# Performance work log

Measured on AMD Instinct MI355X. Metric: run time of the kernel, lower is better.

The kernel has to match this reference:

```python
import jax, jax.numpy as jnp
import numpy as np

B, N_HEADS, KEY_DIM, ATTN_RATIO, RES, DIM = 8, 12, 64, 4, 32, 768
D = ATTN_RATIO * KEY_DIM          # per-head v dim = 256
DH = N_HEADS * D                  # 3072
QKV_OUT = N_HEADS * (2 * KEY_DIM + D)  # 4608
N = RES * RES                     # 1024 tokens
TH = 0.99
WBITS, ABITS, PGABITS = 8, 8, 4


def quantize(x, bits):
    # TorchQuantize: round(x * 2^(b-1)) / 2^(b-1) with straight-through estimator
    s = jnp.asarray(2.0 ** (bits - 1), x.dtype)
    q = jnp.round(x * s) / s
    return x + jax.lax.stop_gradient(q - x)


def ste_greater_than(x, th):
    # GreaterThan: hard (x > th) forward, identity gradient
    hard = (x > th).astype(x.dtype)
    return x + jax.lax.stop_gradient(hard - x)


def hardswish(x):
    return x * jnp.clip(x + 3.0, 0.0, 6.0) / 6.0


def _make_bias_idxs(res):
    pts = np.stack(np.meshgrid(np.arange(res), np.arange(res), indexing='ij'), -1).reshape(-1, 2)
    off = np.abs(pts[:, None, :] - pts[None, :, :])          # [N,N,2]
    key = off[..., 0] * res + off[..., 1]
    uniq, inv = np.unique(key, return_inverse=True)
    return inv.reshape(res * res, res * res).astype(np.int32), len(uniq)


def setup_inputs() -> dict:
    key = jax.random.key(0)
    ks = jax.random.split(key, 8)
    bias_idxs_np, n_uniq = _make_bias_idxs(RES)
    return {
        "x": jax.random.normal(ks[0], (B, N, DIM), jnp.float32),
        "qkv_w": jax.random.normal(ks[1], (QKV_OUT, DIM), jnp.float32) * (DIM ** -0.5),
        "qkv_g": jnp.ones((QKV_OUT,), jnp.float32),
        "qkv_b": jnp.zeros((QKV_OUT,), jnp.float32),
        "proj_w": jax.random.normal(ks[2], (DIM, DH), jnp.float32) * (DH ** -0.5),
        "proj_g": jnp.ones((DIM,), jnp.float32),
        "proj_b": jnp.zeros((DIM,), jnp.float32),
        "attn_biases": jax.random.normal(ks[3], (N_HEADS, n_uniq), jnp.float32) * 0.02,
        "bias_idxs": jnp.asarray(bias_idxs_np),
    }


def reference(x, qkv_w, qkv_g, qkv_b, proj_w, proj_g, proj_b, attn_biases, bias_idxs):
    Bq, Nq, C = x.shape
    scale = KEY_DIM ** -0.5
    # QLinear qkv (8-bit act/weight) followed by fused BN affine (Linear_BN)
    h = quantize(x, ABITS) @ quantize(qkv_w, WBITS).T
    h = h * qkv_g + qkv_b                                     # [B,N,QKV_OUT]
    h = quantize(h, ABITS)
    h = h.reshape(Bq, Nq, N_HEADS, 2 * KEY_DIM + D).transpose(0, 2, 1, 3)  # [B,H,N,*]
    q, k, v = h[..., :KEY_DIM], h[..., KEY_DIM:2 * KEY_DIM], h[..., 2 * KEY_DIM:]
    bias = attn_biases[:, bias_idxs]                          # [H,N,N]
    # MSB (low-precision) predictive attention -> gating mask
    q_msb = quantize(q, PGABITS)
    k_msb = quantize(k, PGABITS)
    attn_msb = jnp.einsum('bhnd,bhmd->bhnm', q_msb, k_msb) * scale + bias
    attn_msb = jax.nn.softmax(attn_msb, axis=-1)
    mask = ste_greater_than(attn_msb, TH)                     # [B,H,N,N]
    # Full-precision attention, threshold-gated (ena_schedule=False)
    attn = jnp.einsum('bhnd,bhmd->bhnm', q, k) * scale + bias
    attn = jax.nn.softmax(attn * mask, axis=-1)
    attn = quantize(attn, ABITS)
    out = jnp.einsum('bhnm,bhmd->bhnd', attn, v)              # [B,H,N,D]
    out = out.transpose(0, 2, 1, 3).reshape(Bq, Nq, DH)
    out = hardswish(out)                                      # proj = Seq(act, Linear_BN)
    out = quantize(out, ABITS) @ quantize(proj_w, WBITS).T
    out = out * proj_g + proj_b                               # [B,N,DIM]
    return out
```

## Files before the change

### kernel.cpp

```cpp
#include <hip/hip_runtime.h>

typedef _Float16 f16;
typedef _Float16 f16x8 __attribute__((ext_vector_type(8)));
typedef _Float16 f16x4 __attribute__((ext_vector_type(4)));
typedef float    f32x4 __attribute__((ext_vector_type(4)));
typedef int      i32x4 __attribute__((ext_vector_type(4)));

#define MFMA16(a,b,c) __builtin_amdgcn_mfma_f32_16x16x32_f16((a),(b),(c),0,0,0)
#define MFMAI8(a,b,c) __builtin_amdgcn_mfma_i32_16x16x64_i8((a),(b),(c),0,0,0)
#define AS1(p) ((const __attribute__((address_space(1))) void*)(p))
#define AS3(p) ((__attribute__((address_space(3))) void*)(p))

constexpr int   NH   = 12;
constexpr int   SEQ  = 1024;
constexpr float INV128 = 1.0f/128.0f;
constexpr int   ECAP = 98304;
constexpr float THR_NOT = -4.5948f;

__device__ __forceinline__ float q8f(float x){ return rintf(x*128.0f)*INV128; }
__device__ __forceinline__ float q4f(float x){ return rintf(x*8.0f)*0.125f; }

__global__ __launch_bounds__(256) void prelude(
    const float* __restrict__ x, const float* __restrict__ qkv_w,
    float* __restrict__ out, const float* __restrict__ pb,
    const float* __restrict__ biases, int NU,
    f16* __restrict__ xq, f16* __restrict__ wqk,
    float* __restrict__ Bh, int* __restrict__ cnt2)
{
    const int b = blockIdx.x, t = threadIdx.x;
    if (b < 6144){
        int i = (b*256 + t)*4;
        float4 v = *(const float4*)(x + i);
        f16x4 o;
        o[0]=(f16)q8f(v.x); o[1]=(f16)q8f(v.y); o[2]=(f16)q8f(v.z); o[3]=(f16)q8f(v.w);
        *(f16x4*)(xq + i) = o;
    } else if (b < 7296){
        int i = ((b-6144)*256 + t)*4;
        int r = i / 768, col = i - r*768;
        int srow = (r>>7)*384 + (r&127);
        float4 v = *(const float4*)(qkv_w + (size_t)srow*768 + col);
        f16x4 o;
        o[0]=(f16)q8f(v.x); o[1]=(f16)q8f(v.y); o[2]=(f16)q8f(v.z); o[3]=(f16)q8f(v.w);
        *(f16x4*)(wqk + i) = o;
    } else if (b < 13440){
        int i = ((b-7296)*256 + t)*4;
        int c = i % 768;
        float4 v = { pb[c], pb[c+1], pb[c+2], pb[c+3] };
        *(float4*)(out + i) = v;
    } else {
        int h = b - 13440;
        float m = 0.f;
        for (int i = t; i < NU; i += 256) m = fmaxf(m, fabsf(biases[h*NU + i]));
        #pragma unroll
        for (int d=32; d>=1; d>>=1) m = fmaxf(m, __shfl_xor(m, d));
        __shared__ float s[4];
        if ((t&63)==0) s[t>>6] = m;
        __syncthreads();
        if (t==0){
            Bh[h] = fmaxf(fmaxf(s[0],s[1]), fmaxf(s[2],s[3]));
            if (h==0) *cnt2 = 0;
        }
    }
}

__global__ __launch_bounds__(256, 2) void gemm_qk(
    const f16* __restrict__ Aq, const f16* __restrict__ Wqk,
    const float* __restrict__ g, const float* __restrict__ bb,
    signed char* __restrict__ Qi, signed char* __restrict__ Ki)
{
    __shared__ f16 As[2][128][64];
    __shared__ f16 Bs[2][192][64];
    const int t = threadIdx.x;
    const int bid = blockIdx.x;
    const int xcd = bid & 7, idx = bid >> 3;
    const int mt  = xcd*8 + (idx >> 3);
    const int nt  = idx & 7;
    const int row0 = mt*128, col0 = nt*192;
    const int w = t>>6, lane = t&63;
    const int wr = (w>>1)*64, wc = (w&1)*96;
    const int lr = lane&15, lg = lane>>4;

    const int rloc  = lane>>3;
    const int sgran = (lane&7) ^ rloc;
    const f16* Abase = Aq  + (size_t)(row0 + w*32 + rloc)*768 + sgran*8;
    const f16* Bbase = Wqk + (size_t)(col0 + w*48 + rloc)*768 + sgran*8;

    f32x4 acc[4][6] = {};

#define STAGE(buf, kt) { \
    const int ko = (kt)*64; \
    __builtin_amdgcn_global_load_lds(AS1(Abase + (size_t) 0*768 + ko), AS3(&As[buf][w*32 +  0][0]), 16, 0, 0); \
    __builtin_amdgcn_global_load_lds(AS1(Abase + (size_t) 8*768 + ko), AS3(&As[buf][w*32 +  8][0]), 16, 0, 0); \
    __builtin_amdgcn_global_load_lds(AS1(Abase + (size_t)16*768 + ko), AS3(&As[buf][w*32 + 16][0]), 16, 0, 0); \
    __builtin_amdgcn_global_load_lds(AS1(Abase + (size_t)24*768 + ko), AS3(&As[buf][w*32 + 24][0]), 16, 0, 0); \
    __builtin_amdgcn_global_load_lds(AS1(Bbase + (size_t) 0*768 + ko), AS3(&Bs[buf][w*48 +  0][0]), 16, 0, 0); \
    __builtin_amdgcn_global_load_lds(AS1(Bbase + (size_t) 8*768 + ko), AS3(&Bs[buf][w*48 +  8][0]), 16, 0, 0); \
    __builtin_amdgcn_global_load_lds(AS1(Bbase + (size_t)16*768 + ko), AS3(&Bs[buf][w*48 + 16][0]), 16, 0, 0); \
    __builtin_amdgcn_global_load_lds(AS1(Bbase + (size_t)24*768 + ko), AS3(&Bs[buf][w*48 + 24][0]), 16, 0, 0); \
    __builtin_amdgcn_global_load_lds(AS1(Bbase + (size_t)32*768 + ko), AS3(&Bs[buf][w*48 + 32][0]), 16, 0, 0); \
    __builtin_amdgcn_global_load_lds(AS1(Bbase + (size_t)40*768 + ko), AS3(&Bs[buf][w*48 + 40][0]), 16, 0, 0); }

    STAGE(0, 0)

    for (int kt = 0; kt < 12; kt++){
        __builtin_amdgcn_s_barrier();
        if (kt < 11){
            STAGE((kt+1)&1, kt+1)
            asm volatile("s_waitcnt vmcnt(10)" ::: "memory");
        } else {
            asm volatile("s_waitcnt vmcnt(0)" ::: "memory");
        }
        __builtin_amdgcn_s_barrier();

        const int bsel = kt & 1;
        #pragma unroll
        for (int kk=0; kk<2; kk++){
            const int slot = ((kk*4 + lg) ^ (lr&7))*8;
            f16x8 af[4], bf[6];
            #pragma unroll
            for (int i=0;i<4;i++)
                af[i] = *(const f16x8*)&As[bsel][wr + i*16 + lr][slot];
            #pragma unroll
            for (int j=0;j<6;j++)
                bf[j] = *(const f16x8*)&Bs[bsel][wc + j*16 + lr][slot];
            __builtin_amdgcn_s_setprio(1);
            #pragma unroll
            for (int i=0;i<4;i++)
                #pragma unroll
                for (int j=0;j<6;j++)
                    acc[i][j] = MFMA16(af[i], bf[j], acc[i][j]);
            __builtin_amdgcn_s_setprio(0);
        }
    }
#undef STAGE

    #pragma unroll
    for (int j=0;j<6;j++){
        int c = col0 + wc + j*16 + lr;
        int head = c >> 7, rr = c & 127;
        int gcol = head*384 + rr;
        float gg = g[gcol], bv = bb[gcol];
        signed char* dst = (rr < 64) ? Qi : Ki;
        int dcol = rr & 63;
        #pragma unroll
        for (int i=0;i<4;i++){
            #pragma unroll
            for (int r=0;r<4;r++){
                int grow = row0 + wr + i*16 + lg*4 + r;
                float h = __fadd_rn(__fmul_rn(acc[i][j][r], gg), bv);
                int iv = (int)rintf(q8f(h)*8.0f);
                int bq = grow >> 10, n = grow & 1023;
                dst[((size_t)(bq*NH + head)*SEQ + n)*64 + dcol] = (signed char)iv;
            }
        }
    }
}

__global__ __launch_bounds__(256) void pass_a(
    const signed char* __restrict__ Qi, const signed char* __restrict__ Ki,
    const float* __restrict__ Bh,
    int* __restrict__ cnt2, int2* __restrict__ amb)
{
    __shared__ signed char Ks[128][64];

    const int t = threadIdx.x;
    const int bid = blockIdx.x;
    const int wg  = (bid & 7)*192 + (bid >> 3);
    const int bh  = wg >> 4;
    const int qt  = wg & 15;
    const int n0 = qt*64;
    const int lane = t&63, w = t>>6;
    const int lr = lane&15, lg = lane>>4;

    const float thr512 = (THR_NOT + 2.0f*Bh[bh % NH] + 1e-4f) * 512.0f;

    const signed char* qp = Qi + ((size_t)bh*SEQ + n0 + w*16 + lr)*64;
    const i32x4 aq = *(const i32x4*)(qp + lg*16);

    const signed char* Kb = Ki + (size_t)bh*SEQ*64;

    int mx[4], m2[4];
    #pragma unroll
    for (int r=0;r<4;r++){ mx[r] = -(1<<30); m2[r] = -(1<<30); }

    for (int kb = 0; kb < SEQ; kb += 128){
        __syncthreads();
        for (int s = t; s < 512; s += 256){
            int r = s>>2, gsw = s&3;
            int src = (gsw ^ (r&3))*16;
            *(i32x4*)&Ks[r][gsw*16] = *(const i32x4*)(Kb + (size_t)(kb + r)*64 + src);
        }
        __syncthreads();
        #pragma unroll
        for (int ct=0; ct<8; ct++){
            const int row = ct*16 + lr;
            i32x4 bq = *(const i32x4*)&Ks[row][(lg ^ (lr&3))*16];
            i32x4 c = {0,0,0,0};
            c = MFMAI8(aq, bq, c);
            #pragma unroll
            for (int r=0;r<4;r++){
                int sc = c[r];
                int om = mx[r];
                asm("v_med3_i32 %0, %1, %2, %3" : "=v"(m2[r]) : "v"(sc), "v"(m2[r]), "v"(om));
                mx[r] = max(om, sc);
            }
        }
    }

    #pragma unroll
    for (int r=0;r<4;r++){
        int mxv = mx[r], m2v = m2[r];
        #pragma unroll
        for (int d=1; d<16; d<<=1){
            int mo  = __shfl_xor(mxv, d);
            int m2o = __shfl_xor(m2v, d);
            int sec = max(min(mxv, mo), (mxv >= mo) ? m2v : m2o);
            mxv = max(mxv, mo);
            m2v = sec;
        }
        if (lr == 0){
            if ((float)(m2v - mxv) < thr512){
                int n = n0 + w*16 + lg*4 + r;
                int pos = atomicAdd(cnt2, 1);
                if (pos < ECAP) amb[pos] = make_int2((bh<<10) | n, 0);
            }
        }
    }
}

__global__ __launch_bounds__(256) void tail_kernel(
    const signed char* __restrict__ Qi, const signed char* __restrict__ Ki,
    const float* __restrict__ biases, int NU,
    const f16* __restrict__ xq, const f16* __restrict__ wqk,
    const float* __restrict__ qkv_w,
    const float* __restrict__ g, const float* __restrict__ bb,
    const float* __restrict__ proj_w, const float* __restrict__ pg,
    const int* __restrict__ cnt2, const int2* __restrict__ amb,
    float* __restrict__ out)
{
    __shared__ int   qr[64];
    __shared__ float rmax[4], rsum[4];
    __shared__ int   rarg[4];
    __shared__ float xr_n[768], xr_m[768];
    __shared__ float qs[64], ks[64];
    __shared__ float hq[256];
    __shared__ float s_as;
    __shared__ int   s_ms, s_flag;
    int total = *cnt2; if (total > ECAP) total = ECAP;
    const int t = threadIdx.x;
    for (int e = blockIdx.x; e < total; e += gridDim.x){
        int2 a = amb[e];
        int bh = a.x>>10, n = a.x&1023;
        int h = bh % NH, b = bh / NH;
        __syncthreads();
        if (t < 64) qr[t] = (int)Qi[((size_t)bh*SEQ + n)*64 + t];
        __syncthreads();

        int rn = n>>5, cnn = n&31;
        float lmax = -3e38f; int larg = 0; float lsc[4];
        #pragma unroll
        for (int j=0;j<4;j++){
            int m = t + j*256;
            const signed char* kp = &Ki[((size_t)bh*SEQ + m)*64];
            int d = 0;
            for (int u=0; u<64; u++) d += qr[u]*(int)kp[u];
            int idx = __builtin_abs(rn-(m>>5))*32 + __builtin_abs(cnn-(m&31));
            lsc[j] = (float)d*(1.0f/512.0f) + biases[h*NU + idx];
            if (lsc[j] > lmax){ lmax = lsc[j]; larg = m; }
        }
        #pragma unroll
        for (int dd=32; dd>=1; dd>>=1){
            float mo = __shfl_xor(lmax, dd);
            int   ao = __shfl_xor(larg, dd);
            if (mo > lmax){ lmax = mo; larg = ao; }
        }
        if ((t&63)==0){ rmax[t>>6] = lmax; rarg[t>>6] = larg; }
        __syncthreads();
        float MX = rmax[0]; int ARG = rarg[0];
        #pragma unroll
        for (int k=1;k<4;k++){ if (rmax[k] > MX){ MX = rmax[k]; ARG = rarg[k]; } }
        float ls = 0.f;
        #pragma unroll
        for (int j=0;j<4;j++) ls += expf(lsc[j]-MX);
        #pragma unroll
        for (int dd=32; dd>=1; dd>>=1) ls += __shfl_xor(ls, dd);
        if ((t&63)==0) rsum[t>>6] = ls;
        __syncthreads();
        if (t==0){
            float SUM = rsum[0]+rsum[1]+rsum[2]+rsum[3];
            s_flag = (1.0f/SUM > 0.99f);
            s_ms = ARG;
        }
        __syncthreads();
        if (!s_flag) continue;
        const int ms = s_ms;

        for (int i=t; i<768; i+=256){
            xr_n[i] = (float)xq[((size_t)b*SEQ + n)*768 + i];
            xr_m[i] = (float)xq[((size_t)b*SEQ + ms)*768 + i];
        }
        __syncthreads();
        if (t < 128){
            int col = t & 63;
            int qkr  = h*128 + (t<64 ? col : 64+col);
            int gcol = h*384 + (t<64 ? col : 64+col);
            const f16* wr = &wqk[(size_t)qkr*768];
            const float* xr = (t<64) ? xr_n : xr_m;
            float acc = 0.f;
            for (int d=0; d<768; d++) acc = fmaf(xr[d], (float)wr[d], acc);
            float hv = __fadd_rn(__fmul_rn(acc, g[gcol]), bb[gcol]);
            float v = q8f(hv);
            if (t<64) qs[col] = v; else ks[col] = v;
        }
        __syncthreads();
        if (t < 64){
            float p = qs[t]*ks[t];
            #pragma unroll
            for (int d=32; d>=1; d>>=1) p += __shfl_xor(p, d);
            if (t == 0){
                int idx = __builtin_abs((n>>5)-(ms>>5))*32 + __builtin_abs((n&31)-(ms&31));
                float ss = __fadd_rn(__fmul_rn(p, 0.125f), biases[h*NU + idx]);
                float mx2 = fmaxf(ss, 0.f);
                float es = expf(ss-mx2), e0 = expf(-mx2);
                float Z = fmaf(1023.f, e0, es);
                s_as = q8f(es/Z);
            }
        }
        __syncthreads();
        {
            int gcol = h*384 + 128 + t;
            const float* wr = &qkv_w[(size_t)gcol*768];
            float acc = 0.f;
            for (int d=0; d<768; d++) acc = fmaf(xr_m[d], q8f(wr[d]), acc);
            float hv = __fadd_rn(__fmul_rn(acc, g[gcol]), bb[gcol]);
            float vq = q8f(hv);
            float o = __fmul_rn(s_as, vq);
            float c6 = fminf(fmaxf(o+3.f, 0.f), 6.f);
            hq[t] = q8f(__fdiv_rn(__fmul_rn(o, c6), 6.f));
        }
        __syncthreads();
        #pragma unroll
        for (int cc=0; cc<3; cc++){
            int c = t + cc*256;
            float s = 0.f;
            for (int d=0; d<256; d++)
                s = fmaf(hq[d], q8f(proj_w[(size_t)c*3072 + h*256 + d]), s);
            atomicAdd(&out[((size_t)b*SEQ + n)*768 + c], __fmul_rn(pg[c], s));
        }
    }
}

extern "C" void kernel_launch(void* const* d_in, const int* in_sizes, int n_in,
                              void* d_out, int out_size, void* d_ws, size_t ws_size,
                              hipStream_t stream)
{
    const float* x       = (const float*)d_in[0];
    const float* qkv_w   = (const float*)d_in[1];
    const float* qkv_g   = (const float*)d_in[2];
    const float* qkv_b   = (const float*)d_in[3];
    const float* proj_w  = (const float*)d_in[4];
    const float* proj_g  = (const float*)d_in[5];
    const float* proj_b  = (const float*)d_in[6];
    const float* biases  = (const float*)d_in[7];
    const int NU = in_sizes[7] / NH;

    char* w = (char*)d_ws;
    f16* xq  = (f16*)w; w += (size_t)8192*768*2;
    f16* wqk = (f16*)w; w += (size_t)1536*768*2;
    signed char* Qi = (signed char*)w; w += (size_t)96*1024*64;
    signed char* Ki = (signed char*)w; w += (size_t)96*1024*64;
    int* cnt2= (int*)w;  w += 16;
    float* Bh = (float*)w; w += 64;
    int2* amb = (int2*)w; w += (size_t)ECAP*8;

    prelude<<<13452, 256, 0, stream>>>(x, qkv_w, (float*)d_out, proj_b, biases, NU,
                                       xq, wqk, Bh, cnt2);

    gemm_qk<<<512, 256, 0, stream>>>(xq, wqk, qkv_g, qkv_b, Qi, Ki);

    pass_a<<<1536, 256, 0, stream>>>(Qi, Ki, Bh, cnt2, amb);

    tail_kernel<<<256, 256, 0, stream>>>(Qi, Ki, biases, NU, xq, wqk, qkv_w,
                                         qkv_g, qkv_b, proj_w, proj_g,
                                         cnt2, amb, (float*)d_out);
}
```

Before: 57.27 us.

## Restructure pass_a to register-blocked Q tiles with direct K loads, no LDS

Each wave now handles 64 query rows (four 16-row MFMA tiles) instead of 16. It streams K straight from global memory into registers with a one-step software prefetch, dropping the shared-memory staging and the __syncthreads barriers. Each K fragment is reused across four MFMAs. The grid shrinks from 1536 to 384 blocks, which cuts redundant K traffic but lowers parallelism and raises register use.

Result: slower. 58.84 us (+2.7%).

```diff
diff --git a/kernel.cpp b/kernel.cpp
--- a/kernel.cpp
+++ b/kernel.cpp
@@ -161,68 +161,69 @@
     const float* __restrict__ Bh,
     int* __restrict__ cnt2, int2* __restrict__ amb)
 {
-    __shared__ signed char Ks[128][64];
-
     const int t = threadIdx.x;
     const int bid = blockIdx.x;
-    const int wg  = (bid & 7)*192 + (bid >> 3);
-    const int bh  = wg >> 4;
-    const int qt  = wg & 15;
-    const int n0 = qt*64;
+    const int wg  = (bid & 7)*48 + (bid >> 3);
+    const int bh  = wg >> 2;
+    const int qq  = wg & 3;
     const int lane = t&63, w = t>>6;
+    const int n0 = qq*256 + w*64;
     const int lr = lane&15, lg = lane>>4;
 
     const float thr512 = (THR_NOT + 2.0f*Bh[bh % NH] + 1e-4f) * 512.0f;
 
-    const signed char* qp = Qi + ((size_t)bh*SEQ + n0 + w*16 + lr)*64;
-    const i32x4 aq = *(const i32x4*)(qp + lg*16);
-
-    const signed char* Kb = Ki + (size_t)bh*SEQ*64;
-
-    int mx[4], m2[4];
+    i32x4 aq[4];
     #pragma unroll
-    for (int r=0;r<4;r++){ mx[r] = -(1<<30); m2[r] = -(1<<30); }
-
-    for (int kb = 0; kb < SEQ; kb += 128){
-        __syncthreads();
-        for (int s = t; s < 512; s += 256){
-            int r = s>>2, gsw = s&3;
-            int src = (gsw ^ (r&3))*16;
-            *(i32x4*)&Ks[r][gsw*16] = *(const i32x4*)(Kb + (size_t)(kb + r)*64 + src);
-        }
-        __syncthreads();
-        #pragma unroll
-        for (int ct=0; ct<8; ct++){
-            const int row = ct*16 + lr;
-            i32x4 bq = *(const i32x4*)&Ks[row][(lg ^ (lr&3))*16];
+    for (int i=0;i<4;i++)
+        aq[i] = *(const i32x4*)(Qi + ((size_t)bh*SEQ + n0 + i*16 + lr)*64 + lg*16);
+
+    const signed char* kp = Ki + (size_t)bh*SEQ*64 + lr*64 + lg*16;
+
+    int mx[4][4], m2[4][4];
+    #pragma unroll
+    for (int i=0;i<4;i++)
+        #pragma unroll
+        for (int r=0;r<4;r++){ mx[i][r] = -(1<<30); m2[i][r] = -(1<<30); }
+
+    i32x4 kbuf = *(const i32x4*)(kp);
+    #pragma unroll 4
+    for (int kb = 0; kb < 1024; kb += 16){
+        i32x4 knext;
+        if (kb < 1008) knext = *(const i32x4*)(kp + (size_t)(kb+16)*64);
+        #pragma unroll
+        for (int i=0;i<4;i++){
             i32x4 c = {0,0,0,0};
-            c = MFMAI8(aq, bq, c);
+            c = MFMAI8(aq[i], kbuf, c);
             #pragma unroll
             for (int r=0;r<4;r++){
                 int sc = c[r];
-                int om = mx[r];
-                asm("v_med3_i32 %0, %1, %2, %3" : "=v"(m2[r]) : "v"(sc), "v"(m2[r]), "v"(om));
-                mx[r] = max(om, sc);
-            }
-        }
+                int om = mx[i][r];
+                asm("v_med3_i32 %0, %1, %2, %3" : "=v"(m2[i][r]) : "v"(sc), "v"(m2[i][r]), "v"(om));
+                mx[i][r] = max(om, sc);
+            }
+        }
+        kbuf = knext;
     }
 
     #pragma unroll
-    for (int r=0;r<4;r++){
-        int mxv = mx[r], m2v = m2[r];
-        #pragma unroll
-        for (int d=1; d<16; d<<=1){
-            int mo  = __shfl_xor(mxv, d);
-            int m2o = __shfl_xor(m2v, d);
-            int sec = max(min(mxv, mo), (mxv >= mo) ? m2v : m2o);
-            mxv = max(mxv, mo);
-            m2v = sec;
-        }
-        if (lr == 0){
-            if ((float)(m2v - mxv) < thr512){
-                int n = n0 + w*16 + lg*4 + r;
-                int pos = atomicAdd(cnt2, 1);
-                if (pos < ECAP) amb[pos] = make_int2((bh<<10) | n, 0);
+    for (int i=0;i<4;i++){
+        #pragma unroll
+        for (int r=0;r<4;r++){
+            int mxv = mx[i][r], m2v = m2[i][r];
+            #pragma unroll
+            for (int d=1; d<16; d<<=1){
+                int mo  = __shfl_xor(mxv, d);
+                int m2o = __shfl_xor(m2v, d);
+                int sec = max(min(mxv, mo), (mxv >= mo) ? m2v : m2o);
+                mxv = max(mxv, mo);
+                m2v = sec;
+            }
+            if (lr == 0){
+                if ((float)(m2v - mxv) < thr512){
+                    int n = n0 + i*16 + lg*4 + r;
+                    int pos = atomicAdd(cnt2, 1);
+                    if (pos < ECAP) amb[pos] = make_int2((bh<<10) | n, 0);
+                }
             }
         }
     }
@@ -378,7 +379,7 @@
 
     gemm_qk<<<512, 256, 0, stream>>>(xq, wqk, qkv_g, qkv_b, Qi, Ki);
 
-    pass_a<<<1536, 256, 0, stream>>>(Qi, Ki, Bh, cnt2, amb);
+    pass_a<<<384, 256, 0, stream>>>(Qi, Ki, Bh, cnt2, amb);
 
     tail_kernel<<<256, 256, 0, stream>>>(Qi, Ki, biases, NU, xq, wqk, qkv_w,
                                          qkv_g, qkv_b, proj_w, proj_g,
```
